# Performance work log

Hardware: AMD Instinct MI355X
Metric: run time of the kernel (lower is better)

## Reference

```python
import jax, jax.numpy as jnp
import numpy as np

N = 10000
E = 160000
B = 16
NEG_SLOPE = 0.2


def gat_conv(x, src, dst, W, a_src, a_dst, b, heads, ch):
    # x: [N, F_in]; src/dst: [E'] (self-loops included); W: [F_in, heads*ch]
    n = x.shape[0]
    h = (x @ W).reshape(n, heads, ch)                     # [N,H,C]
    alpha_src = jnp.sum(h * a_src, axis=-1)               # [N,H]
    alpha_dst = jnp.sum(h * a_dst, axis=-1)               # [N,H]
    e = jax.nn.leaky_relu(alpha_src[src] + alpha_dst[dst], NEG_SLOPE)  # [E,H]
    # segment softmax over edges grouped by destination node
    m = jax.ops.segment_max(e, dst, num_segments=n)       # [N,H]
    ex = jnp.exp(e - m[dst])                              # [E,H]
    denom = jax.ops.segment_sum(ex, dst, num_segments=n)  # [N,H]
    alpha = ex / denom[dst]                               # [E,H]
    out = jax.ops.segment_sum(alpha[:, :, None] * h[src], dst, num_segments=n)  # [N,H,C]
    return out.reshape(n, heads * ch) + b


def setup_inputs() -> dict:
    key = jax.random.key(0)
    ks = jax.random.split(key, 16)
    glorot = lambda k, shp: jax.random.normal(k, shp, jnp.float32) * np.sqrt(2.0 / (shp[0] + shp[-1]))
    inp = {
        "x": jax.random.normal(ks[0], (N, 128), jnp.float32),
        "edge_index": jax.random.randint(ks[1], (2, E), 0, N, jnp.int64),
        "batch": jnp.sort(jax.random.randint(ks[2], (N,), 0, B, jnp.int64)),
        # conv1: 128 -> 128 per head, 8 heads
        "W1": glorot(ks[3], (128, 8 * 128)),
        "att_src1": glorot(ks[4], (8, 128)),
        "att_dst1": glorot(ks[5], (8, 128)),
        "b1": jnp.zeros((8 * 128,), jnp.float32),
        # conv2: 1024 -> 64 per head, 8 heads
        "W2": glorot(ks[6], (1024, 8 * 64)),
        "att_src2": glorot(ks[7], (8, 64)),
        "att_dst2": glorot(ks[8], (8, 64)),
        "b2": jnp.zeros((8 * 64,), jnp.float32),
        "fc1_w": glorot(ks[9], (512, 32)),
        "fc1_b": jnp.zeros((32,), jnp.float32),
        "fc2_w": glorot(ks[10], (32, 10)),
        "fc2_b": jnp.zeros((10,), jnp.float32),
    }
    return inp


def reference(x, edge_index, batch, W1, att_src1, att_dst1, b1,
              W2, att_src2, att_dst2, b2, fc1_w, fc1_b, fc2_w, fc2_b):
    n = x.shape[0]
    loop = jnp.arange(n, dtype=edge_index.dtype)
    src = jnp.concatenate([edge_index[0], loop])  # PyG add_self_loops=True
    dst = jnp.concatenate([edge_index[1], loop])
    h = jax.nn.elu(gat_conv(x, src, dst, W1, att_src1, att_dst1, b1, 8, 128))   # [N,1024]
    h = jax.nn.elu(gat_conv(h, src, dst, W2, att_src2, att_dst2, b2, 8, 64))    # [N,512]
    # global mean pool over graphs
    sums = jax.ops.segment_sum(h, batch, num_segments=B)                        # [B,512]
    cnt = jax.ops.segment_sum(jnp.ones((n,), h.dtype), batch, num_segments=B)
    g = sums / jnp.maximum(cnt, 1.0)[:, None]
    g = jax.nn.elu(g @ fc1_w + fc1_b)
    return g @ fc2_w + fc2_b                                                    # [B,10]
```

## Files before the change

### kernel.cpp

```cpp
#include <hip/hip_runtime.h>
#include <math.h>

#define HEADS 8
#define NEG 0.2f

typedef unsigned short ushort_t;
typedef __attribute__((ext_vector_type(8))) short short8;
typedef float f32x4 __attribute__((ext_vector_type(4)));

__device__ inline ushort_t f2bf(float f) {
  union { float f; unsigned u; } v; v.f = f;
  unsigned r = (v.u + 0x7FFF + ((v.u >> 16) & 1)) >> 16;
  return (ushort_t)r;
}

__device__ inline float4 bf4(uint2 v) {
  union { unsigned u; float f; } a, b, c, d;
  a.u = v.x << 16; b.u = v.x & 0xffff0000u;
  c.u = v.y << 16; d.u = v.y & 0xffff0000u;
  return make_float4(a.f, b.f, c.f, d.f);
}

__device__ inline float elu_f(float v) {
  return (v > 0.f) ? v : (__expf(v) - 1.f);
}

#define GLDS16(gp, lp)                                                          \
  __builtin_amdgcn_global_load_lds(                                             \
      (const __attribute__((address_space(1))) void*)(gp),                      \
      (__attribute__((address_space(3))) void*)(lp), 16, 0, 0)

__global__ __launch_bounds__(256) void init_k(int* __restrict__ ws, int zero_words,
                                              const float* __restrict__ x,
                                              ushort_t* __restrict__ xb,
                                              const float* __restrict__ W1,
                                              ushort_t* __restrict__ w1t,
                                              const float* __restrict__ W2,
                                              ushort_t* __restrict__ w2t, int nx4) {
  __shared__ float tile[32][33];
  int blk = blockIdx.x;
  if (blk < 640) {
    const float* W; ushort_t* Wt; int K, N, tk, tn;
    if (blk < 128) { W = W1; Wt = w1t; K = 128; N = 1024; tk = blk >> 5; tn = blk & 31; }
    else { W = W2; Wt = w2t; K = 1024; N = 512; int t = blk - 128; tk = t >> 4; tn = t & 15; }
    int tx = threadIdx.x & 31, ty = threadIdx.x >> 5;
    int k0 = tk * 32, n0 = tn * 32;
#pragma unroll
    for (int r = 0; r < 4; r++)
      tile[ty + r * 8][tx] = W[(size_t)(k0 + ty + r * 8) * N + n0 + tx];
    __syncthreads();
#pragma unroll
    for (int r = 0; r < 4; r++)
      Wt[(size_t)(n0 + ty + r * 8) * K + k0 + tx] = f2bf(tile[tx][ty + r * 8]);
  } else {
    int i = (blk - 640) * 256 + threadIdx.x;
    if (i < zero_words) ws[i] = 0;
    if (i < nx4) {
      float4 v = ((const float4*)x)[i];
      ushort_t o[4] = {f2bf(v.x), f2bf(v.y), f2bf(v.z), f2bf(v.w)};
      *(uint2*)&xb[i * 4] = *(uint2*)o;
    }
  }
}

__global__ void prep_k(const int* __restrict__ ei, int* __restrict__ src,
                       int* __restrict__ dst, int* __restrict__ deg,
                       const int* __restrict__ batch, int* __restrict__ bstart,
                       int* __restrict__ bend, int E, int Nn) {
  int i = blockIdx.x * blockDim.x + threadIdx.x;
  if (i < Nn) {
    int b = batch[i];
    if (i == 0 || batch[i - 1] != b) bstart[b] = i;
    if (i == Nn - 1 || batch[i + 1] != b) bend[b] = i + 1;
  }
  if (i >= E + Nn) return;
  int s, d;
  if (i < E) { s = ei[i]; d = ei[E + i]; }
  else       { s = d = i - E; }
  src[i] = s;
  dst[i] = d;
  atomicAdd(&deg[d], 1);
}

__global__ __launch_bounds__(1024) void scan_k(const int* __restrict__ deg,
                                               int* __restrict__ offs,
                                               int* __restrict__ cursor, int Nn) {
  __shared__ int wtot[16];
  __shared__ int wexcl[16];
  __shared__ int soff_s;
  int t = threadIdx.x;
  int lane = t & 63, w = t >> 6;
  if (t == 0) soff_s = 0;
  __syncthreads();
  for (int base = 0; base < Nn; base += 4096) {
    int idx = base + 4 * t;
    int4 v = make_int4(0, 0, 0, 0);
    if (idx + 3 < Nn) v = *(const int4*)&deg[idx];
    else {
      if (idx < Nn)     v.x = deg[idx];
      if (idx + 1 < Nn) v.y = deg[idx + 1];
      if (idx + 2 < Nn) v.z = deg[idx + 2];
      if (idx + 3 < Nn) v.w = deg[idx + 3];
    }
    int s1 = v.x, s2 = s1 + v.y, s3 = s2 + v.z, s4 = s3 + v.w;
    int sc = s4;
#pragma unroll
    for (int o = 1; o < 64; o <<= 1) {
      int x = __shfl_up(sc, o);
      if (lane >= o) sc += x;
    }
    if (lane == 63) wtot[w] = sc;
    __syncthreads();
    if (w == 0) {
      int tv = (lane < 16) ? wtot[lane] : 0;
      int ts = tv;
#pragma unroll
      for (int o = 1; o < 16; o <<= 1) {
        int x = __shfl_up(ts, o);
        if (lane >= o) ts += x;
      }
      if (lane < 16) wexcl[lane] = ts - tv;
      if (lane == 15) wtot[15] = ts;
    }
    __syncthreads();
    int excl = soff_s + wexcl[w] + (sc - s4);
    int o0 = excl, o1 = excl + s1, o2 = excl + s2, o3 = excl + s3;
    if (idx < Nn)     { offs[idx] = o0;     cursor[idx] = o0; }
    if (idx + 1 < Nn) { offs[idx + 1] = o1; cursor[idx + 1] = o1; }
    if (idx + 2 < Nn) { offs[idx + 2] = o2; cursor[idx + 2] = o2; }
    if (idx + 3 < Nn) { offs[idx + 3] = o3; cursor[idx + 3] = o3; }
    int chunk_total = wtot[15];
    __syncthreads();
    if (t == 0) soff_s += chunk_total;
    __syncthreads();
  }
  if (t == 0) offs[Nn] = soff_s;
}

__global__ void scatter_k(const int* __restrict__ src, const int* __restrict__ dst,
                          int* __restrict__ cursor, int* __restrict__ psrc, int Etot) {
  int i = blockIdx.x * blockDim.x + threadIdx.x;
  if (i >= Etot) return;
  int p = atomicAdd(&cursor[dst[i]], 1);
  psrc[p] = src[i];
}

__global__ __launch_bounds__(256) void pa_k(const float* __restrict__ W1,
                                            const float* __restrict__ as1,
                                            const float* __restrict__ ad1,
                                            float* __restrict__ Ps,
                                            float* __restrict__ Pd) {
  int h = blockIdx.x;
  int t = threadIdx.x;
  int k = t >> 1, sd = t & 1;
  const float* att = sd ? ad1 : as1;
  float* P = sd ? Pd : Ps;
  const float* wrow = &W1[(size_t)k * 1024 + h * 128];
  const float* arow = &att[h * 128];
  float s = 0.f;
#pragma unroll 8
  for (int c = 0; c < 128; c++) s += wrow[c] * arow[c];
  P[k * 8 + h] = s;
}

__global__ __launch_bounds__(256) void al1_k(const float* __restrict__ x,
                                             const float* __restrict__ Ps,
                                             const float* __restrict__ Pd,
                                             float* __restrict__ asrc,
                                             float* __restrict__ adst, int Nn) {
  __shared__ float ps[1024], pd[1024];
  int t = threadIdx.x;
  for (int i = t; i < 1024; i += 256) { ps[i] = Ps[i]; pd[i] = Pd[i]; }
  __syncthreads();
  int n = blockIdx.x * 256 + t;
  if (n >= Nn) return;
  const float4* xr = (const float4*)&x[(size_t)n * 128];
  float as[8], ad[8];
#pragma unroll
  for (int h = 0; h < 8; h++) { as[h] = 0.f; ad[h] = 0.f; }
  for (int k4 = 0; k4 < 32; k4++) {
    float4 xv = xr[k4];
    float xs[4] = {xv.x, xv.y, xv.z, xv.w};
#pragma unroll
    for (int j = 0; j < 4; j++) {
      int k = k4 * 4 + j;
#pragma unroll
      for (int h = 0; h < 8; h++) {
        as[h] += xs[j] * ps[k * 8 + h];
        ad[h] += xs[j] * pd[k * 8 + h];
      }
    }
  }
#pragma unroll
  for (int h = 0; h < 8; h++) {
    asrc[n * 8 + h] = as[h];
    adst[n * 8 + h] = ad[h];
  }
}

__global__ __launch_bounds__(64) void aggx_k(const ushort_t* __restrict__ xb,
                                             const float* __restrict__ asrc,
                                             const float* __restrict__ adst,
                                             const int* __restrict__ offs,
                                             const int* __restrict__ psrc,
                                             ushort_t* __restrict__ sb, int Nn) {
  int n = blockIdx.x;
  int l = threadIdx.x;
  int u_mine = l >> 3, h_mine = l & 7;
  float adn = adst[n * 8 + h_mine];
  int e0 = offs[n], e1 = offs[n + 1];
  int c0 = l * 2;
  float acc0[8], acc1[8], wsum[8];
#pragma unroll
  for (int h = 0; h < 8; h++) { acc0[h] = 0.f; acc1[h] = 0.f; wsum[h] = 0.f; }

  for (int i = e0; i < e1; i += 8) {
    int bs = min(8, e1 - i);
    int eu = i + (u_mine < bs ? u_mine : bs - 1);
    int se = psrc[eu];
    float v = asrc[se * 8 + h_mine] + adn;
    v = (v > 0.f) ? v : NEG * v;
    float wm = __expf(v);
    int ss[8];
    unsigned xvv[8];
#pragma unroll
    for (int u = 0; u < 8; u++) ss[u] = psrc[i + (u < bs ? u : bs - 1)];
#pragma unroll
    for (int u = 0; u < 8; u++) xvv[u] = *(const unsigned*)&xb[(size_t)ss[u] * 128 + c0];
#pragma unroll
    for (int u = 0; u < 8; u++) {
      if (u < bs) {
        union { unsigned u; float f; } a, b;
        a.u = xvv[u] << 16; b.u = xvv[u] & 0xffff0000u;
#pragma unroll
        for (int h = 0; h < 8; h++) {
          float w = __shfl(wm, (u << 3) | h);
          acc0[h] += w * a.f;
          acc1[h] += w * b.f;
          wsum[h] += w;
        }
      }
    }
  }

#pragma unroll
  for (int h = 0; h < 8; h++) {
    float inv = 1.f / wsum[h];
    unsigned pr = (unsigned)f2bf(acc0[h] * inv) | ((unsigned)f2bf(acc1[h] * inv) << 16);
    *(unsigned*)&sb[(size_t)n * 1024 + h * 128 + c0] = pr;
  }
}

__global__ __launch_bounds__(256) void hgemm_k(const ushort_t* __restrict__ S,
                                               const ushort_t* __restrict__ Wt,
                                               const float* __restrict__ bias,
                                               ushort_t* __restrict__ G, int M) {
  __shared__ __attribute__((aligned(16))) ushort_t lds[32768];
  int tid = threadIdx.x;
  int lane = tid & 63;
  int wave = tid >> 6;
  int wm = (wave >> 1) * 64, wn = (wave & 1) * 64;
  int head = blockIdx.x;
  int hb0 = head * 128;
  int bm = blockIdx.y * 128;
  int lrow = lane & 15, lq = lane >> 4;

  f32x4 acc[4][4];
#pragma unroll
  for (int i = 0; i < 4; i++)
#pragma unroll
    for (int j = 0; j < 4; j++) acc[i][j] = 0.f;

  int srow = lane >> 3;
  int scol = 8 * ((lane & 7) ^ srow);
  const ushort_t* pa[4];
  const ushort_t* pb[4];
  int lofs[4];
#pragma unroll
  for (int c = 0; c < 4; c++) {
    int row = wave * 32 + c * 8 + srow;
    int ga = min(bm + row, M - 1);
    pa[c] = &S[(size_t)ga * 1024 + hb0 + scol];
    pb[c] = &Wt[(size_t)(hb0 + row) * 128 + scol];
    lofs[c] = (wave * 4 + c) * 512;
  }

  auto stage = [&](int buf, int k0) {
#pragma unroll
    for (int c = 0; c < 4; c++) GLDS16(pa[c] + k0, &lds[buf * 8192 + lofs[c]]);
#pragma unroll
    for (int c = 0; c < 4; c++) GLDS16(pb[c] + k0, &lds[16384 + buf * 8192 + lofs[c]]);
  };
  auto compute = [&](int buf) {
    const ushort_t* Asb = &lds[buf * 8192];
    const ushort_t* Bsb = &lds[16384 + buf * 8192];
#pragma unroll
    for (int ks = 0; ks < 2; ks++) {
      short8 af[4], bfr[4];
#pragma unroll
      for (int t = 0; t < 4; t++) {
        int cbs = (ks * 64 + lq * 16) ^ ((lrow & 7) << 4);
        af[t]  = *(const short8*)&Asb[(wm + t * 16 + lrow) * 64 + (cbs >> 1)];
        bfr[t] = *(const short8*)&Bsb[(wn + t * 16 + lrow) * 64 + (cbs >> 1)];
      }
#pragma unroll
      for (int i = 0; i < 4; i++)
#pragma unroll
        for (int j = 0; j < 4; j++)
          acc[i][j] = __builtin_amdgcn_mfma_f32_16x16x32_bf16(af[i], bfr[j], acc[i][j], 0, 0, 0);
    }
  };

  stage(0, 0);
  asm volatile("s_waitcnt vmcnt(0)" ::: "memory");
  __builtin_amdgcn_s_barrier();
  stage(1, 64);
  compute(0);
  asm volatile("s_waitcnt vmcnt(0)" ::: "memory");
  __builtin_amdgcn_s_barrier();
  compute(1);

  __syncthreads();

  ushort_t* Cl = lds;
  float bv[4];
#pragma unroll
  for (int j = 0; j < 4; j++) bv[j] = bias[hb0 + wn + j * 16 + lrow];
#pragma unroll
  for (int i = 0; i < 4; i++) {
#pragma unroll
    for (int j = 0; j < 4; j++) {
      int col = wn + j * 16 + lrow;
#pragma unroll
      for (int r = 0; r < 4; r++) {
        int row = wm + i * 16 + lq * 4 + r;
        Cl[row * 136 + col] = f2bf(elu_f(acc[i][j][r] + bv[j]));
      }
    }
  }
  __syncthreads();
#pragma unroll
  for (int p = 0; p < 8; p++) {
    int row = p * 16 + (tid >> 4);
    int col8 = (tid & 15) * 8;
    if (bm + row < M)
      *(uint4*)&G[(size_t)(bm + row) * 1024 + hb0 + col8] = *(const uint4*)&Cl[row * 136 + col8];
  }
}

__global__ __launch_bounds__(256) void mfma_gemm_k(const ushort_t* __restrict__ A,
                                                   const ushort_t* __restrict__ Bt,
                                                   ushort_t* __restrict__ Cb,
                                                   const float* __restrict__ att_s,
                                                   const float* __restrict__ att_d,
                                                   float* __restrict__ asrc,
                                                   float* __restrict__ adst,
                                                   int M, int N, int K, int CSHIFT) {
  __shared__ __attribute__((aligned(16))) ushort_t lds[32768];
  int tid = threadIdx.x;
  int lane = tid & 63;
  int wave = tid >> 6;
  int wm = (wave >> 1) * 64, wn = (wave & 1) * 64;
  int bm = blockIdx.y * 128, bn = blockIdx.x * 128;
  int lrow = lane & 15, lq = lane >> 4;

  f32x4 acc[4][4];
#pragma unroll
  for (int i = 0; i < 4; i++)
#pragma unroll
    for (int j = 0; j < 4; j++) acc[i][j] = 0.f;

  int srow = lane >> 3;
  int scol = 8 * ((lane & 7) ^ srow);
  const ushort_t* pa[4];
  const ushort_t* pb[4];
  int lofs[4];
#pragma unroll
  for (int c = 0; c < 4; c++) {
    int row = wave * 32 + c * 8 + srow;
    int ga = min(bm + row, M - 1);
    pa[c] = &A[(size_t)ga * K + scol];
    pb[c] = &Bt[(size_t)(bn + row) * K + scol];
    lofs[c] = (wave * 4 + c) * 512;
  }

  auto stage = [&](int buf, int k0) {
#pragma unroll
    for (int c = 0; c < 4; c++) GLDS16(pa[c] + k0, &lds[buf * 8192 + lofs[c]]);
#pragma unroll
    for (int c = 0; c < 4; c++) GLDS16(pb[c] + k0, &lds[16384 + buf * 8192 + lofs[c]]);
  };
  auto compute = [&](int buf) {
    const ushort_t* Asb = &lds[buf * 8192];
    const ushort_t* Bsb = &lds[16384 + buf * 8192];
#pragma unroll
    for (int ks = 0; ks < 2; ks++) {
      short8 af[4], bfr[4];
#pragma unroll
      for (int t = 0; t < 4; t++) {
        int cbs = (ks * 64 + lq * 16) ^ ((lrow & 7) << 4);
        af[t]  = *(const short8*)&Asb[(wm + t * 16 + lrow) * 64 + (cbs >> 1)];
        bfr[t] = *(const short8*)&Bsb[(wn + t * 16 + lrow) * 64 + (cbs >> 1)];
      }
#pragma unroll
      for (int i = 0; i < 4; i++)
#pragma unroll
        for (int j = 0; j < 4; j++)
          acc[i][j] = __builtin_amdgcn_mfma_f32_16x16x32_bf16(af[i], bfr[j], acc[i][j], 0, 0, 0);
    }
  };

  int NT = K >> 6;
  stage(0, 0);
  asm volatile("s_waitcnt vmcnt(0)" ::: "memory");
  __builtin_amdgcn_s_barrier();
  int cur = 0;
  for (int t = 0; t + 1 < NT; ++t) {
    stage(cur ^ 1, (t + 1) << 6);
    compute(cur);
    asm volatile("s_waitcnt vmcnt(0)" ::: "memory");
    __builtin_amdgcn_s_barrier();
    cur ^= 1;
  }
  compute(cur);

  __syncthreads();

  ushort_t* Cl = lds;
  float* pls = (float*)&lds[17472];
  float* pld = pls + 256;

  {
    float avs[4], avd[4];
#pragma unroll
    for (int j = 0; j < 4; j++) {
      int col = bn + wn + j * 16 + lrow;
      avs[j] = att_s[col];
      avd[j] = att_d[col];
    }
#pragma unroll
    for (int i = 0; i < 4; i++) {
#pragma unroll
      for (int r = 0; r < 4; r++) {
        float ps = 0.f, pd = 0.f;
#pragma unroll
        for (int j = 0; j < 4; j++) {
          float v = acc[i][j][r];
          ps += v * avs[j];
          pd += v * avd[j];
        }
#pragma unroll
        for (int o = 1; o < 16; o <<= 1) {
          ps += __shfl_xor(ps, o);
          pd += __shfl_xor(pd, o);
        }
        if (lrow == 0) {
          int rr = i * 16 + lq * 4 + r;
          pls[wave * 64 + rr] = ps;
          pld[wave * 64 + rr] = pd;
        }
      }
    }
  }

#pragma unroll
  for (int i = 0; i < 4; i++) {
#pragma unroll
    for (int j = 0; j < 4; j++) {
      int col = wn + j * 16 + lrow;
#pragma unroll
      for (int r = 0; r < 4; r++) {
        int row = wm + i * 16 + lq * 4 + r;
        Cl[row * 136 + col] = f2bf(acc[i][j][r]);
      }
    }
  }
  __syncthreads();

#pragma unroll
  for (int p = 0; p < 8; p++) {
    int row = p * 16 + (tid >> 4);
    int col8 = (tid & 15) * 8;
    if (bm + row < M)
      *(uint4*)&Cb[(size_t)(bm + row) * N + bn + col8] = *(const uint4*)&Cl[row * 136 + col8];
  }

  {
    int r = tid & 127, half = tid >> 7;
    if (bm + r < M) {
      const float* P = half ? pld : pls;
      float* O = half ? adst : asrc;
      int w0 = (r >> 6) * 2, idx = r & 63;
      float va = P[w0 * 64 + idx];
      float vb = P[(w0 + 1) * 64 + idx];
      int h0 = bn >> CSHIFT, h1 = (bn + 64) >> CSHIFT;
      size_t base = (size_t)(bm + r) * HEADS;
      if (h0 == h1) O[base + h0] = va + vb;
      else { O[base + h0] = va; O[base + h1] = vb; }
    }
  }
}

template <int F, int CSHIFT, int BT, int NSPLIT, typename OT>
__global__ __launch_bounds__(BT) void aggregate_k(const ushort_t* __restrict__ hb,
                                                  const float* __restrict__ asrc,
                                                  const float* __restrict__ adst,
                                                  const int* __restrict__ offs,
                                                  const int* __restrict__ psrc,
                                                  const float* __restrict__ bias,
                                                  OT* __restrict__ out) {
  constexpr int CPB = F / NSPLIT;
  constexpr int G = (1 << CSHIFT) >> 2;
  static_assert(CPB == 4 * BT, "CPB/thread mismatch");
  static_assert(G >= 8 && G <= 64, "head group must cover the 8-edge batch");
  int nb = blockIdx.x;
  int n = nb / NSPLIT;
  int coff = (nb - n * NSPLIT) * CPB;
  int t = threadIdx.x;
  int c0 = coff + 4 * t;
  int hh = c0 >> CSHIFT;
  int lane = t & 63;
  int sub = lane & (G - 1);
  int gb = lane & ~(G - 1);
  float adn = adst[n * HEADS + hh];
  int e0 = offs[n], e1 = offs[n + 1];
  float4 acc = make_float4(0.f, 0.f, 0.f, 0.f);
  float wsum = 0.f;

  int i = e0;
  uint2 rA[8];
  float myWA = 0.f;
  bool haveA = (i + 8 <= e1);
  if (haveA) {
    int sA[8];
#pragma unroll
    for (int u = 0; u < 8; u++) sA[u] = psrc[i + u];
#pragma unroll
    for (int u = 0; u < 8; u++) rA[u] = *(const uint2*)&hb[(size_t)sA[u] * F + c0];
    int ms = psrc[i + (sub < 8 ? sub : 0)];
    float v = asrc[ms * HEADS + hh] + adn;
    v = (v > 0.f) ? v : NEG * v;
    myWA = __expf(v);
  }
  while (i + 16 <= e1) {
    int sB[8];
    uint2 rB[8];
#pragma unroll
    for (int u = 0; u < 8; u++) sB[u] = psrc[i + 8 + u];
#pragma unroll
    for (int u = 0; u < 8; u++) rB[u] = *(const uint2*)&hb[(size_t)sB[u] * F + c0];
    int ms = psrc[i + 8 + (sub < 8 ? sub : 0)];
    float vb = asrc[ms * HEADS + hh] + adn;
    vb = (vb > 0.f) ? vb : NEG * vb;
    float myWB = __expf(vb);
#pragma unroll
    for (int u = 0; u < 8; u++) {
      float w = __shfl(myWA, gb + u);
      float4 f = bf4(rA[u]);
      wsum += w;
      acc.x += w * f.x;
      acc.y += w * f.y;
      acc.z += w * f.z;
      acc.w += w * f.w;
    }
    i += 8;
#pragma unroll
    for (int u = 0; u < 8; u++) rA[u] = rB[u];
    myWA = myWB;
  }
  if (haveA) {
#pragma unroll
    for (int u = 0; u < 8; u++) {
      float w = __shfl(myWA, gb + u);
      float4 f = bf4(rA[u]);
      wsum += w;
      acc.x += w * f.x;
      acc.y += w * f.y;
      acc.z += w * f.z;
      acc.w += w * f.w;
    }
    i += 8;
  }
  for (; i < e1; i++) {
    int ss = psrc[i];
    float v = asrc[ss * HEADS + hh] + adn;
    v = (v > 0.f) ? v : NEG * v;
    float w = __expf(v);
    float4 f = bf4(*(const uint2*)&hb[(size_t)ss * F + c0]);
    wsum += w;
    acc.x += w * f.x; acc.y += w * f.y;
    acc.z += w * f.z; acc.w += w * f.w;
  }

  float inv = 1.f / wsum;
  float v0 = elu_f(acc.x * inv + bias[c0]);
  float v1 = elu_f(acc.y * inv + bias[c0 + 1]);
  float v2 = elu_f(acc.z * inv + bias[c0 + 2]);
  float v3 = elu_f(acc.w * inv + bias[c0 + 3]);
  if constexpr (sizeof(OT) == 2) {
    unsigned p0 = (unsigned)f2bf(v0) | ((unsigned)f2bf(v1) << 16);
    unsigned p1 = (unsigned)f2bf(v2) | ((unsigned)f2bf(v3) << 16);
    *(uint2*)&((ushort_t*)out)[(size_t)n * F + c0] = make_uint2(p0, p1);
  } else {
    *(float4*)&((float*)out)[(size_t)n * F + c0] = make_float4(v0, v1, v2, v3);
  }
}

__global__ __launch_bounds__(256) void pool_k(const float* __restrict__ g,
                                              const int* __restrict__ batch,
                                              float* __restrict__ sums, int Nn) {
  int c = blockIdx.x * 256 + threadIdx.x;
  int n0 = blockIdx.y * 50;
  int n1 = min(n0 + 50, Nn);
  if (n0 >= n1) return;
  float acc = 0.f;
  int cur = batch[n0];
  for (int n = n0; n < n1; n++) {
    int b = batch[n];
    if (b != cur) { atomicAdd(&sums[cur * 512 + c], acc); acc = 0.f; cur = b; }
    acc += g[(size_t)n * 512 + c];
  }
  atomicAdd(&sums[cur * 512 + c], acc);
}

__global__ __launch_bounds__(512) void mlp_k(const float* __restrict__ sums,
                                             const int* __restrict__ bstart,
                                             const int* __restrict__ bend,
                                             const float* __restrict__ w1,
                                             const float* __restrict__ b1,
                                             const float* __restrict__ w2,
                                             const float* __restrict__ b2,
                                             float* __restrict__ out) {
  __shared__ float gm[16 * 512];
  __shared__ float t1[16 * 32];
  int t = threadIdx.x;
  for (int i = t; i < 16 * 512; i += 512) {
    int b = i >> 9;
    float c = (float)(bend[b] - bstart[b]);
    gm[i] = sums[i] / fmaxf(c, 1.f);
  }
  __syncthreads();
  {
    int b = t >> 5, j = t & 31;
    float s = b1[j];
    for (int k = 0; k < 512; k++) s += gm[(b << 9) + k] * w1[k * 32 + j];
    t1[t] = elu_f(s);
  }
  __syncthreads();
  if (t < 160) {
    int b = t / 10, j = t - b * 10;
    float s = b2[j];
#pragma unroll
    for (int k = 0; k < 32; k++) s += t1[b * 32 + k] * w2[k * 10 + j];
    out[t] = s;
  }
}

extern "C" void kernel_launch(void* const* d_in, const int* in_sizes, int n_in,
                              void* d_out, int out_size, void* d_ws, size_t ws_size,
                              hipStream_t stream) {
  const float* x   = (const float*)d_in[0];
  const int*   ei  = (const int*)d_in[1];
  const int* batch = (const int*)d_in[2];
  const float* W1  = (const float*)d_in[3];
  const float* as1 = (const float*)d_in[4];
  const float* ad1 = (const float*)d_in[5];
  const float* b1  = (const float*)d_in[6];
  const float* W2  = (const float*)d_in[7];
  const float* as2 = (const float*)d_in[8];
  const float* ad2 = (const float*)d_in[9];
  const float* b2  = (const float*)d_in[10];
  const float* f1w = (const float*)d_in[11];
  const float* f1b = (const float*)d_in[12];
  const float* f2w = (const float*)d_in[13];
  const float* f2b = (const float*)d_in[14];
  float* out = (float*)d_out;

  const int Nn = in_sizes[2];
  const int E = in_sizes[1] / 2;
  const int Etot = E + Nn;

  size_t off = 0;
  auto alloc = [&](size_t elems) { size_t o = off; off += (elems + 63) & ~(size_t)63; return o; };
  int* wsi = (int*)d_ws;
  float* wsf = (float*)d_ws;

  size_t o_deg  = alloc(Nn);
  size_t o_pool = alloc(16 * 512);
  size_t zero_words = off;
  size_t o_as1  = alloc((size_t)Nn * 8);
  size_t o_ad1  = alloc((size_t)Nn * 8);
  size_t o_as2  = alloc((size_t)Nn * 8);
  size_t o_ad2  = alloc((size_t)Nn * 8);
  size_t o_ps   = alloc(1024);
  size_t o_pd   = alloc(1024);
  size_t o_bst  = alloc(64);
  size_t o_ben  = alloc(64);
  size_t o_offs = alloc(Nn + 1);
  size_t o_cur  = alloc(Nn);
  size_t o_src  = alloc(Etot);
  size_t o_dst  = alloc(Etot);
  size_t o_psrc = alloc(Etot);
  size_t o_xb   = alloc((size_t)Nn * 128 / 2);
  size_t o_w1t  = alloc(1024 * 128 / 2);
  size_t o_w2t  = alloc(512 * 1024 / 2);
  size_t o_s    = alloc((size_t)Nn * 1024 / 2);
  size_t o_h    = alloc((size_t)Nn * 1024 / 2);
  size_t o_g    = alloc((size_t)Nn * 1024);

  ushort_t* xb  = (ushort_t*)(wsi + o_xb);
  ushort_t* w1t = (ushort_t*)(wsi + o_w1t);
  ushort_t* w2t = (ushort_t*)(wsi + o_w2t);
  ushort_t* sb  = (ushort_t*)(wsi + o_s);
  ushort_t* hb  = (ushort_t*)(wsi + o_h);
  ushort_t* g1b = (ushort_t*)(wsi + o_g);

  int eb = (Etot + 255) / 256;

  int nx4 = Nn * 128 / 4;
  int ep_work = (int)((zero_words > (size_t)nx4 ? zero_words : (size_t)nx4));
  int init_blocks = 640 + (ep_work + 255) / 256;
  init_k<<<init_blocks, 256, 0, stream>>>(wsi, (int)zero_words, x, xb,
                                          W1, w1t, W2, w2t, nx4);
  prep_k<<<eb, 256, 0, stream>>>(ei, wsi + o_src, wsi + o_dst, wsi + o_deg,
                                 batch, wsi + o_bst, wsi + o_ben, E, Nn);
  scan_k<<<1, 1024, 0, stream>>>(wsi + o_deg, wsi + o_offs, wsi + o_cur, Nn);
  scatter_k<<<eb, 256, 0, stream>>>(wsi + o_src, wsi + o_dst, wsi + o_cur,
                                    wsi + o_psrc, Etot);

  pa_k<<<8, 256, 0, stream>>>(W1, as1, ad1, wsf + o_ps, wsf + o_pd);
  al1_k<<<(Nn + 255) / 256, 256, 0, stream>>>(x, wsf + o_ps, wsf + o_pd,
                                              wsf + o_as1, wsf + o_ad1, Nn);
  aggx_k<<<Nn, 64, 0, stream>>>(xb, wsf + o_as1, wsf + o_ad1,
                                wsi + o_offs, wsi + o_psrc, sb, Nn);
  hgemm_k<<<dim3(8, (Nn + 127) / 128), 256, 0, stream>>>(sb, w1t, b1, g1b, Nn);

  mfma_gemm_k<<<dim3(512 / 128, (Nn + 127) / 128), 256, 0, stream>>>(
      g1b, w2t, hb, as2, ad2, wsf + o_as2, wsf + o_ad2, Nn, 512, 1024, 6);
  aggregate_k<512, 6, 64, 2, float><<<Nn * 2, 64, 0, stream>>>(
      hb, wsf + o_as2, wsf + o_ad2, wsi + o_offs, wsi + o_psrc, b2, wsf + o_g);

  pool_k<<<dim3(2, (Nn + 49) / 50), 256, 0, stream>>>(wsf + o_g, batch, wsf + o_pool, Nn);
  mlp_k<<<1, 512, 0, stream>>>(wsf + o_pool, wsi + o_bst, wsi + o_ben, f1w, f1b, f2w, f2b, out);
}
```

Baseline: 249.7 us.

## Fold small kernels into init/scatter launches and narrow layer-2 GEMM tiles

Moves the attention-projection precompute into extra blocks of the init kernel and the per-node layer-1 alpha computation into extra blocks of the scatter kernel, removing two kernel launches. Separately, the layer-2 MFMA GEMM tile is narrowed from 128x128 to 128x64 so the grid doubles (8x79 blocks), improving CU occupancy for the small M; each block's output tile now lies within a single head, which simplifies the alpha epilogue. Narrower tiles mean A is re-read more often, and the merged blocks share one launch's shared-memory allocation.

```diff
diff --git a/kernel.cpp b/kernel.cpp
--- a/kernel.cpp
+++ b/kernel.cpp
@@ -36,7 +36,11 @@
                                               const float* __restrict__ W1,
                                               ushort_t* __restrict__ w1t,
                                               const float* __restrict__ W2,
-                                              ushort_t* __restrict__ w2t, int nx4) {
+                                              ushort_t* __restrict__ w2t,
+                                              const float* __restrict__ as1,
+                                              const float* __restrict__ ad1,
+                                              float* __restrict__ Ps,
+                                              float* __restrict__ Pd, int nx4) {
   __shared__ float tile[32][33];
   int blk = blockIdx.x;
   if (blk < 640) {
@@ -52,8 +56,20 @@
 #pragma unroll
     for (int r = 0; r < 4; r++)
       Wt[(size_t)(n0 + ty + r * 8) * K + k0 + tx] = f2bf(tile[tx][ty + r * 8]);
+  } else if (blk < 648) {
+    int h = blk - 640;
+    int t = threadIdx.x;
+    int k = t >> 1, sd = t & 1;
+    const float* att = sd ? ad1 : as1;
+    float* P = sd ? Pd : Ps;
+    const float* wrow = &W1[(size_t)k * 1024 + h * 128];
+    const float* arow = &att[h * 128];
+    float s = 0.f;
+#pragma unroll 8
+    for (int c = 0; c < 128; c++) s += wrow[c] * arow[c];
+    P[k * 8 + h] = s;
   } else {
-    int i = (blk - 640) * 256 + threadIdx.x;
+    int i = (blk - 648) * 256 + threadIdx.x;
     if (i < zero_words) ws[i] = 0;
     if (i < nx4) {
       float4 v = ((const float4*)x)[i];
@@ -137,65 +153,50 @@
   if (t == 0) offs[Nn] = soff_s;
 }
 
-__global__ void scatter_k(const int* __restrict__ src, const int* __restrict__ dst,
-                          int* __restrict__ cursor, int* __restrict__ psrc, int Etot) {
-  int i = blockIdx.x * blockDim.x + threadIdx.x;
+__global__ __launch_bounds__(256) void scatter_k(const int* __restrict__ src,
+                                                 const int* __restrict__ dst,
+                                                 int* __restrict__ cursor,
+                                                 int* __restrict__ psrc, int Etot, int eb,
+                                                 const float* __restrict__ x,
+                                                 const float* __restrict__ Ps,
+                                                 const float* __restrict__ Pd,
+                                                 float* __restrict__ asrc,
+                                                 float* __restrict__ adst, int Nn) {
+  if ((int)blockIdx.x >= eb) {
+    __shared__ float ps[1024], pd[1024];
+    int t = threadIdx.x;
+    for (int i = t; i < 1024; i += 256) { ps[i] = Ps[i]; pd[i] = Pd[i]; }
+    __syncthreads();
+    int n = (blockIdx.x - eb) * 256 + t;
+    if (n >= Nn) return;
+    const float4* xr = (const float4*)&x[(size_t)n * 128];
+    float as[8], ad[8];
+#pragma unroll
+    for (int h = 0; h < 8; h++) { as[h] = 0.f; ad[h] = 0.f; }
+    for (int k4 = 0; k4 < 32; k4++) {
+      float4 xv = xr[k4];
+      float xs[4] = {xv.x, xv.y, xv.z, xv.w};
+#pragma unroll
+      for (int j = 0; j < 4; j++) {
+        int k = k4 * 4 + j;
+#pragma unroll
+        for (int h = 0; h < 8; h++) {
+          as[h] += xs[j] * ps[k * 8 + h];
+          ad[h] += xs[j] * pd[k * 8 + h];
+        }
+      }
+    }
+#pragma unroll
+    for (int h = 0; h < 8; h++) {
+      asrc[n * 8 + h] = as[h];
+      adst[n * 8 + h] = ad[h];
+    }
+    return;
+  }
+  int i = blockIdx.x * 256 + threadIdx.x;
   if (i >= Etot) return;
   int p = atomicAdd(&cursor[dst[i]], 1);
   psrc[p] = src[i];
-}
-
-__global__ __launch_bounds__(256) void pa_k(const float* __restrict__ W1,
-                                            const float* __restrict__ as1,
-                                            const float* __restrict__ ad1,
-                                            float* __restrict__ Ps,
-                                            float* __restrict__ Pd) {
-  int h = blockIdx.x;
-  int t = threadIdx.x;
-  int k = t >> 1, sd = t & 1;
-  const float* att = sd ? ad1 : as1;
-  float* P = sd ? Pd : Ps;
-  const float* wrow = &W1[(size_t)k * 1024 + h * 128];
-  const float* arow = &att[h * 128];
-  float s = 0.f;
-#pragma unroll 8
-  for (int c = 0; c < 128; c++) s += wrow[c] * arow[c];
-  P[k * 8 + h] = s;
-}
-
-__global__ __launch_bounds__(256) void al1_k(const float* __restrict__ x,
-                                             const float* __restrict__ Ps,
-                                             const float* __restrict__ Pd,
-                                             float* __restrict__ asrc,
-                                             float* __restrict__ adst, int Nn) {
-  __shared__ float ps[1024], pd[1024];
-  int t = threadIdx.x;
-  for (int i = t; i < 1024; i += 256) { ps[i] = Ps[i]; pd[i] = Pd[i]; }
-  __syncthreads();
-  int n = blockIdx.x * 256 + t;
-  if (n >= Nn) return;
-  const float4* xr = (const float4*)&x[(size_t)n * 128];
-  float as[8], ad[8];
-#pragma unroll
-  for (int h = 0; h < 8; h++) { as[h] = 0.f; ad[h] = 0.f; }
-  for (int k4 = 0; k4 < 32; k4++) {
-    float4 xv = xr[k4];
-    float xs[4] = {xv.x, xv.y, xv.z, xv.w};
-#pragma unroll
-    for (int j = 0; j < 4; j++) {
-      int k = k4 * 4 + j;
-#pragma unroll
-      for (int h = 0; h < 8; h++) {
-        as[h] += xs[j] * ps[k * 8 + h];
-        ad[h] += xs[j] * pd[k * 8 + h];
-      }
-    }
-  }
-#pragma unroll
-  for (int h = 0; h < 8; h++) {
-    asrc[n * 8 + h] = as[h];
-    adst[n * 8 + h] = ad[h];
-  }
 }
 
 __global__ __launch_bounds__(64) void aggx_k(const ushort_t* __restrict__ xb,
@@ -356,56 +357,63 @@
                                                    float* __restrict__ asrc,
                                                    float* __restrict__ adst,
                                                    int M, int N, int K, int CSHIFT) {
-  __shared__ __attribute__((aligned(16))) ushort_t lds[32768];
+  __shared__ __attribute__((aligned(16))) ushort_t lds[24576];
   int tid = threadIdx.x;
   int lane = tid & 63;
   int wave = tid >> 6;
-  int wm = (wave >> 1) * 64, wn = (wave & 1) * 64;
-  int bm = blockIdx.y * 128, bn = blockIdx.x * 128;
+  int wm = (wave >> 1) * 64, wn = (wave & 1) * 32;
+  int bm = blockIdx.y * 128, bn = blockIdx.x * 64;
   int lrow = lane & 15, lq = lane >> 4;
 
-  f32x4 acc[4][4];
+  f32x4 acc[4][2];
 #pragma unroll
   for (int i = 0; i < 4; i++)
 #pragma unroll
-    for (int j = 0; j < 4; j++) acc[i][j] = 0.f;
+    for (int j = 0; j < 2; j++) acc[i][j] = 0.f;
 
   int srow = lane >> 3;
   int scol = 8 * ((lane & 7) ^ srow);
   const ushort_t* pa[4];
-  const ushort_t* pb[4];
-  int lofs[4];
+  int laofs[4];
 #pragma unroll
   for (int c = 0; c < 4; c++) {
     int row = wave * 32 + c * 8 + srow;
     int ga = min(bm + row, M - 1);
     pa[c] = &A[(size_t)ga * K + scol];
+    laofs[c] = (wave * 4 + c) * 512;
+  }
+  const ushort_t* pb[2];
+  int lbofs[2];
+#pragma unroll
+  for (int c = 0; c < 2; c++) {
+    int row = wave * 16 + c * 8 + srow;
     pb[c] = &Bt[(size_t)(bn + row) * K + scol];
-    lofs[c] = (wave * 4 + c) * 512;
+    lbofs[c] = (wave * 2 + c) * 512;
   }
 
   auto stage = [&](int buf, int k0) {
 #pragma unroll
-    for (int c = 0; c < 4; c++) GLDS16(pa[c] + k0, &lds[buf * 8192 + lofs[c]]);
-#pragma unroll
-    for (int c = 0; c < 4; c++) GLDS16(pb[c] + k0, &lds[16384 + buf * 8192 + lofs[c]]);
+    for (int c = 0; c < 4; c++) GLDS16(pa[c] + k0, &lds[buf * 8192 + laofs[c]]);
+#pragma unroll
+    for (int c = 0; c < 2; c++) GLDS16(pb[c] + k0, &lds[16384 + buf * 4096 + lbofs[c]]);
   };
   auto compute = [&](int buf) {
     const ushort_t* Asb = &lds[buf * 8192];
-    const ushort_t* Bsb = &lds[16384 + buf * 8192];
+    const ushort_t* Bsb = &lds[16384 + buf * 4096];
 #pragma unroll
     for (int ks = 0; ks < 2; ks++) {
-      short8 af[4], bfr[4];
-#pragma unroll
-      for (int t = 0; t < 4; t++) {
-        int cbs = (ks * 64 + lq * 16) ^ ((lrow & 7) << 4);
+      int cbs = (ks * 64 + lq * 16) ^ ((lrow & 7) << 4);
+      short8 af[4], bfr[2];
+#pragma unroll
+      for (int t = 0; t < 4; t++)
         af[t]  = *(const short8*)&Asb[(wm + t * 16 + lrow) * 64 + (cbs >> 1)];
+#pragma unroll
+      for (int t = 0; t < 2; t++)
         bfr[t] = *(const short8*)&Bsb[(wn + t * 16 + lrow) * 64 + (cbs >> 1)];
-      }
 #pragma unroll
       for (int i = 0; i < 4; i++)
 #pragma unroll
-        for (int j = 0; j < 4; j++)
+        for (int j = 0; j < 2; j++)
           acc[i][j] = __builtin_amdgcn_mfma_f32_16x16x32_bf16(af[i], bfr[j], acc[i][j], 0, 0, 0);
     }
   };
@@ -427,13 +435,14 @@
   __syncthreads();
 
   ushort_t* Cl = lds;
-  float* pls = (float*)&lds[17472];
+  float* pls = (float*)&lds[20480];
   float* pld = pls + 256;
 
+  int hh = bn >> CSHIFT;
   {
-    float avs[4], avd[4];
-#pragma unroll
-    for (int j = 0; j < 4; j++) {
+    float avs[2], avd[2];
+#pragma unroll
+    for (int j = 0; j < 2; j++) {
       int col = bn + wn + j * 16 + lrow;
       avs[j] = att_s[col];
       avd[j] = att_d[col];
@@ -444,7 +453,7 @@
       for (int r = 0; r < 4; r++) {
         float ps = 0.f, pd = 0.f;
 #pragma unroll
-        for (int j = 0; j < 4; j++) {
+        for (int j = 0; j < 2; j++) {
           float v = acc[i][j][r];
           ps += v * avs[j];
           pd += v * avd[j];
@@ -466,23 +475,23 @@
 #pragma unroll
   for (int i = 0; i < 4; i++) {
 #pragma unroll
-    for (int j = 0; j < 4; j++) {
+    for (int j = 0; j < 2; j++) {
       int col = wn + j * 16 + lrow;
 #pragma unroll
       for (int r = 0; r < 4; r++) {
         int row = wm + i * 16 + lq * 4 + r;
-        Cl[row * 136 + col] = f2bf(acc[i][j][r]);
+        Cl[row * 72 + col] = f2bf(acc[i][j][r]);
       }
     }
   }
   __syncthreads();
 
 #pragma unroll
-  for (int p = 0; p < 8; p++) {
-    int row = p * 16 + (tid >> 4);
-    int col8 = (tid & 15) * 8;
+  for (int p = 0; p < 4; p++) {
+    int row = p * 32 + (tid >> 3);
+    int col8 = (tid & 7) * 8;
     if (bm + row < M)
-      *(uint4*)&Cb[(size_t)(bm + row) * N + bn + col8] = *(const uint4*)&Cl[row * 136 + col8];
+      *(uint4*)&Cb[(size_t)(bm + row) * N + bn + col8] = *(const uint4*)&Cl[row * 72 + col8];
   }
 
   {
@@ -491,12 +500,7 @@
       const float* P = half ? pld : pls;
       float* O = half ? adst : asrc;
       int w0 = (r >> 6) * 2, idx = r & 63;
-      float va = P[w0 * 64 + idx];
-      float vb = P[(w0 + 1) * 64 + idx];
-      int h0 = bn >> CSHIFT, h1 = (bn + 64) >> CSHIFT;
-      size_t base = (size_t)(bm + r) * HEADS;
-      if (h0 == h1) O[base + h0] = va + vb;
-      else { O[base + h0] = va; O[base + h1] = vb; }
+      O[(size_t)(bm + r) * HEADS + hh] = P[w0 * 64 + idx] + P[(w0 + 1) * 64 + idx];
     }
   }
 }
@@ -716,26 +720,27 @@
   ushort_t* g1b = (ushort_t*)(wsi + o_g);
 
   int eb = (Etot + 255) / 256;
+  int ab = (Nn + 255) / 256;
 
   int nx4 = Nn * 128 / 4;
   int ep_work = (int)((zero_words > (size_t)nx4 ? zero_words : (size_t)nx4));
-  int init_blocks = 640 + (ep_work + 255) / 256;
+  int init_blocks = 648 + (ep_work + 255) / 256;
   init_k<<<init_blocks, 256, 0, stream>>>(wsi, (int)zero_words, x, xb,
-                                          W1, w1t, W2, w2t, nx4);
+                                          W1, w1t, W2, w2t,
+                                          as1, ad1, wsf + o_ps, wsf + o_pd, nx4);
   prep_k<<<eb, 256, 0, stream>>>(ei, wsi + o_src, wsi + o_dst, wsi + o_deg,
                                  batch, wsi + o_bst, wsi + o_ben, E, Nn);
   scan_k<<<1, 1024, 0, stream>>>(wsi + o_deg, wsi + o_offs, wsi + o_cur, Nn);
-  scatter_k<<<eb, 256, 0, stream>>>(wsi + o_src, wsi + o_dst, wsi + o_cur,
-                                    wsi + o_psrc, Etot);
-
-  pa_k<<<8, 256, 0, stream>>>(W1, as1, ad1, wsf + o_ps, wsf + o_pd);
-  al1_k<<<(Nn + 255) / 256, 256, 0, stream>>>(x, wsf + o_ps, wsf + o_pd,
-                                              wsf + o_as1, wsf + o_ad1, Nn);
+  scatter_k<<<eb + ab, 256, 0, stream>>>(wsi + o_src, wsi + o_dst, wsi + o_cur,
+                                         wsi + o_psrc, Etot, eb,
+                                         x, wsf + o_ps, wsf + o_pd,
+                                         wsf + o_as1, wsf + o_ad1, Nn);
+
   aggx_k<<<Nn, 64, 0, stream>>>(xb, wsf + o_as1, wsf + o_ad1,
                                 wsi + o_offs, wsi + o_psrc, sb, Nn);
   hgemm_k<<<dim3(8, (Nn + 127) / 128), 256, 0, stream>>>(sb, w1t, b1, g1b, Nn);
 
-  mfma_gemm_k<<<dim3(512 / 128, (Nn + 127) / 128), 256, 0, stream>>>(
+  mfma_gemm_k<<<dim3(512 / 64, (Nn + 127) / 128), 256, 0, stream>>>(
       g1b, w2t, hb, as2, ad2, wsf + o_as2, wsf + o_ad2, Nn, 512, 1024, 6);
   aggregate_k<512, 6, 64, 2, float><<<Nn * 2, 64, 0, stream>>>(
       hb, wsf + o_as2, wsf + o_ad2, wsi + o_offs, wsi + o_psrc, b2, wsf + o_g);
```

Measured after the change: 251.2 us. Within noise of the previous version (+0.6%).
